# Kernel optimization log

Hardware: AMD Instinct MI355X
Metric: run time of the kernel (lower is better)

The kernel has to match this reference:

```python
import jax, jax.numpy as jnp
import numpy as np

N, A, D = 8192, 512, 512
NN = 3  # n_neighbors


def setup_inputs() -> dict:
    key = jax.random.key(0)
    ks = jax.random.split(key, 7)
    emb = jax.random.normal(ks[0], (N, D), jnp.float32)
    embedding = emb / jnp.linalg.norm(emb, axis=-1, keepdims=True)
    anc = jax.random.normal(ks[1], (A, D), jnp.float32)
    anchors = anc / jnp.linalg.norm(anc, axis=-1, keepdims=True)
    tri = 2.0 * jax.random.uniform(ks[2], (N, A), jnp.float32)  # 1 - cos in [0,2]
    # gate MLP params (Linear(3,16) -> GELU -> Linear(16,1)).
    # NOTE: original init zeros W2 / bias=2.0; random weights used here so the
    # reference exercises nontrivial compute. b2 kept at the module's +2.0.
    W1 = jax.random.normal(ks[3], (16, 3), jnp.float32) * 0.5
    b1 = jax.random.normal(ks[4], (16,), jnp.float32) * 0.1
    W2 = jax.random.normal(ks[5], (1, 16), jnp.float32) * 0.1
    b2 = jnp.full((1,), 2.0, jnp.float32)
    return {"embedding": embedding, "anchors": anchors, "tri": tri,
            "W1": W1, "b1": b1, "W2": W2, "b2": b2}


def _anchor_neighborhood_cm(anchors):
    # pairwise euclidean distances (A,A) with self excluded
    g = anchors @ anchors.T
    sq = jnp.diag(g)
    d2_full = jnp.maximum(sq[:, None] + sq[None, :] - 2.0 * g, 0.0)
    dists = jnp.sqrt(d2_full) + jnp.eye(A, dtype=anchors.dtype) * 1e12
    nn_idx = jnp.argsort(dists, axis=-1)[:, :NN]                       # (A, NN)
    simplices = jnp.concatenate([anchors[:, None, :], anchors[nn_idx]], axis=1)  # (A,K,D)
    K = NN + 1
    # batched pairwise squared distances within each simplex
    gram = jnp.einsum('aid,ajd->aij', simplices, simplices)            # (A,K,K)
    diag = jnp.diagonal(gram, axis1=-2, axis2=-1)
    d2 = diag[:, :, None] + diag[:, None, :] - 2.0 * gram
    # Cayley-Menger matrix (A, K+1, K+1)
    M = jnp.zeros((A, K + 1, K + 1), anchors.dtype)
    M = M.at[:, 0, 1:].set(1.0)
    M = M.at[:, 1:, 0].set(1.0)
    M = M.at[:, 1:, 1:].set(d2)
    raw = jnp.linalg.det(M)
    sign_corr = (-1.0) ** K  # k = K-1, sign = (-1)^(k+1); K=4 -> +1
    dets = sign_corr * raw
    quality = jnp.sign(dets) * jnp.log(jnp.abs(dets) + 1e-12)
    return quality


def reference(embedding, anchors, tri, W1, b1, W2, b2):
    n, a = tri.shape
    anchor_cm = _anchor_neighborhood_cm(anchors)                        # (A,)
    cm_std = jnp.maximum(jnp.std(anchor_cm, ddof=1), 1e-8)
    anchor_cm_norm = (anchor_cm - jnp.mean(anchor_cm)) / cm_std
    cos_sim = 1.0 - tri                                                 # (N,A)
    ranks = jnp.argsort(jnp.argsort(tri, axis=-1), axis=-1).astype(tri.dtype)
    ranks = ranks / max(a - 1, 1)
    feats = jnp.stack([jnp.broadcast_to(anchor_cm_norm[None, :], (n, a)),
                       cos_sim, ranks], axis=-1)                        # (N,A,3)
    h = jax.nn.gelu(jnp.einsum('nac,hc->nah', feats, W1) + b1, approximate=False)
    logits = jnp.einsum('nah,oh->nao', h, W2)[..., 0] + b2[0]           # (N,A)
    return jax.nn.sigmoid(logits)
```

## Files before the change

### kernel.cpp

```cpp
#include <hip/hip_runtime.h>
#include <hip/hip_bf16.h>
#include <math.h>

#define N_ 8192
#define A_ 512
#define D_ 512
#define NN_ 3
#define KPARTS 4

__device__ __forceinline__ float gelu_poly(float x) {
  const float u  = x * x;
  const float s  = fminf(u, 9.0f);
  float p = fmaf(-2.8012e-4f, s, 6.4615e-3f);
  p = fmaf(p, s, -6.1073e-2f);
  p = fmaf(p, s, 3.96693e-1f);
  p = p * s;
  const float ax   = fabsf(x);
  const float e    = fminf(p, 0.5f * ax);
  const float tail = fmaxf(ax - 3.0f, 0.0f);
  return fmaf(0.5f, x, fmaf(0.5f, tail, e));
}

__global__ __launch_bounds__(64) void sq_kernel(
    const float* __restrict__ anchors, float* __restrict__ sq) {
  const int i = blockIdx.x;
  const int l = threadIdx.x;
  const float4* a = reinterpret_cast<const float4*>(anchors + (size_t)i * D_);
  float s = 0.f;
  for (int k = l; k < D_ / 4; k += 64) {
    float4 v = a[k];
    s += v.x * v.x + v.y * v.y + v.z * v.z + v.w * v.w;
  }
#pragma unroll
  for (int d = 32; d > 0; d >>= 1) s += __shfl_down(s, d);
  if (l == 0) sq[i] = s;
}

__global__ __launch_bounds__(256) void gram_tiled_kernel(
    const float* __restrict__ anchors, float* __restrict__ G) {
  __shared__ float At[32][68];
  __shared__ float Bt[32][68];

  const int tx = threadIdx.x;
  const int ty = threadIdx.y;
  const int tid = ty * 16 + tx;
  const int i0 = blockIdx.y * 64;
  const int j0 = blockIdx.x * 64;
  const int z  = blockIdx.z;
  float* Gz = G + (size_t)z * A_ * A_;

  const int r0 = tid >> 3;
  const int c4 = tid & 7;

  float acc[4][4];
#pragma unroll
  for (int m = 0; m < 4; ++m)
#pragma unroll
    for (int n = 0; n < 4; ++n) acc[m][n] = 0.f;

  for (int kt = z * (16 / KPARTS); kt < (z + 1) * (16 / KPARTS); ++kt) {
    const int kb = kt * 32 + c4 * 4;
    float4 va = *reinterpret_cast<const float4*>(&anchors[(size_t)(i0 + r0) * D_ + kb]);
    float4 vb = *reinterpret_cast<const float4*>(&anchors[(size_t)(i0 + r0 + 32) * D_ + kb]);
    float4 wa = *reinterpret_cast<const float4*>(&anchors[(size_t)(j0 + r0) * D_ + kb]);
    float4 wb = *reinterpret_cast<const float4*>(&anchors[(size_t)(j0 + r0 + 32) * D_ + kb]);
    __syncthreads();
    const int kc = c4 * 4;
    At[kc + 0][r0] = va.x; At[kc + 1][r0] = va.y; At[kc + 2][r0] = va.z; At[kc + 3][r0] = va.w;
    At[kc + 0][r0 + 32] = vb.x; At[kc + 1][r0 + 32] = vb.y; At[kc + 2][r0 + 32] = vb.z; At[kc + 3][r0 + 32] = vb.w;
    Bt[kc + 0][r0] = wa.x; Bt[kc + 1][r0] = wa.y; Bt[kc + 2][r0] = wa.z; Bt[kc + 3][r0] = wa.w;
    Bt[kc + 0][r0 + 32] = wb.x; Bt[kc + 1][r0 + 32] = wb.y; Bt[kc + 2][r0 + 32] = wb.z; Bt[kc + 3][r0 + 32] = wb.w;
    __syncthreads();

#pragma unroll
    for (int kk = 0; kk < 32; ++kk) {
      float4 a = *reinterpret_cast<const float4*>(&At[kk][ty * 4]);
      float4 b = *reinterpret_cast<const float4*>(&Bt[kk][tx * 4]);
      acc[0][0] += a.x * b.x; acc[0][1] += a.x * b.y; acc[0][2] += a.x * b.z; acc[0][3] += a.x * b.w;
      acc[1][0] += a.y * b.x; acc[1][1] += a.y * b.y; acc[1][2] += a.y * b.z; acc[1][3] += a.y * b.w;
      acc[2][0] += a.z * b.x; acc[2][1] += a.z * b.y; acc[2][2] += a.z * b.z; acc[2][3] += a.z * b.w;
      acc[3][0] += a.w * b.x; acc[3][1] += a.w * b.y; acc[3][2] += a.w * b.z; acc[3][3] += a.w * b.w;
    }
  }

#pragma unroll
  for (int m = 0; m < 4; ++m) {
    float4 st;
    st.x = acc[m][0]; st.y = acc[m][1]; st.z = acc[m][2]; st.w = acc[m][3];
    *reinterpret_cast<float4*>(&Gz[(size_t)(i0 + ty * 4 + m) * A_ + j0 + tx * 4]) = st;
  }
}

__device__ __forceinline__ void lexmin(float& v, int& j, float ov, int oj) {
  if (ov < v || (ov == v && oj < j)) { v = ov; j = oj; }
}

__global__ __launch_bounds__(64) void nn_det_kernel(
    const float* __restrict__ G, const float* __restrict__ sq,
    float* __restrict__ quality) {
  __shared__ float d2s[16];
  const int i = blockIdx.x;
  const int l = threadIdx.x;
  const float sqi = sq[i];
  const int jb = l * 8;

  float gg[8] = {0.f, 0.f, 0.f, 0.f, 0.f, 0.f, 0.f, 0.f};
#pragma unroll
  for (int z = 0; z < KPARTS; ++z) {
    const float* Grow = G + (size_t)z * A_ * A_ + (size_t)i * A_;
    float4 g0 = *reinterpret_cast<const float4*>(&Grow[jb]);
    float4 g1 = *reinterpret_cast<const float4*>(&Grow[jb + 4]);
    gg[0] += g0.x; gg[1] += g0.y; gg[2] += g0.z; gg[3] += g0.w;
    gg[4] += g1.x; gg[5] += g1.y; gg[6] += g1.z; gg[7] += g1.w;
  }
  float4 s0 = *reinterpret_cast<const float4*>(&sq[jb]);
  float4 s1 = *reinterpret_cast<const float4*>(&sq[jb + 4]);
  float ss[8] = { s0.x, s0.y, s0.z, s0.w, s1.x, s1.y, s1.z, s1.w };

  float dist[8];
#pragma unroll
  for (int q = 0; q < 8; ++q) {
    float d2 = fmaxf(sqi + ss[q] - 2.f * gg[q], 0.f);
    float dd = sqrtf(d2);
    if (jb + q == i) dd += 1e12f;
    dist[q] = dd;
  }

  int nn[NN_];
#pragma unroll
  for (int r = 0; r < NN_; ++r) {
    float bv = 1e30f;
    int bi = 0x7fffffff;
#pragma unroll
    for (int q = 0; q < 8; ++q) lexmin(bv, bi, dist[q], jb + q);
#pragma unroll
    for (int d = 1; d < 64; d <<= 1) {
      float ov = __shfl_xor(bv, d);
      int oi = __shfl_xor(bi, d);
      lexmin(bv, bi, ov, oi);
    }
    nn[r] = bi;
#pragma unroll
    for (int q = 0; q < 8; ++q)
      if (jb + q == bi) dist[q] = 1e30f;
  }

  if (l < 16) {
    const int p = l >> 2, q = l & 3;
    const int pi = (p == 0) ? i : ((p == 1) ? nn[0] : ((p == 2) ? nn[1] : nn[2]));
    const int qi = (q == 0) ? i : ((q == 1) ? nn[0] : ((q == 2) ? nn[1] : nn[2]));
    float d2f;
    if (p == q) {
      d2f = 0.f;
    } else {
      float g = 0.f;
#pragma unroll
      for (int z = 0; z < KPARTS; ++z)
        g += G[(size_t)z * A_ * A_ + (size_t)pi * A_ + qi];
      d2f = sq[pi] + sq[qi] - 2.f * g;
    }
    d2s[l] = d2f;
  }
  __syncthreads();

  if (l == 0) {
    double M[5][5];
    M[0][0] = 0.0;
    for (int q = 1; q < 5; ++q) { M[0][q] = 1.0; M[q][0] = 1.0; }
    for (int p = 0; p < 4; ++p)
      for (int q = 0; q < 4; ++q)
        M[p + 1][q + 1] = (double)d2s[p * 4 + q];

    double det = 1.0;
    for (int c = 0; c < 5; ++c) {
      int piv = c;
      double mx = fabs(M[c][c]);
      for (int r2 = c + 1; r2 < 5; ++r2) {
        double v = fabs(M[r2][c]);
        if (v > mx) { mx = v; piv = r2; }
      }
      if (piv != c) {
        for (int c2 = 0; c2 < 5; ++c2) { double tmp = M[c][c2]; M[c][c2] = M[piv][c2]; M[piv][c2] = tmp; }
        det = -det;
      }
      double pv = M[c][c];
      det *= pv;
      if (pv == 0.0) break;
      for (int r2 = c + 1; r2 < 5; ++r2) {
        double f = M[r2][c] / pv;
        for (int c2 = c; c2 < 5; ++c2) M[r2][c2] -= f * M[c][c2];
      }
    }
    float raw = (float)det;
    float sg = (raw > 0.f) ? 1.f : ((raw < 0.f) ? -1.f : 0.f);
    quality[i] = sg * logf(fabsf(raw) + 1e-12f);
  }
}

__global__ __launch_bounds__(A_) void norm_cm_kernel(
    const float* __restrict__ quality, float* __restrict__ cmn) {
  __shared__ float red[A_];
  const int t = threadIdx.x;
  float q = quality[t];
  red[t] = q;
  __syncthreads();
  for (int s = A_ / 2; s > 0; s >>= 1) {
    if (t < s) red[t] += red[t + s];
    __syncthreads();
  }
  float mean = red[0] * (1.0f / A_);
  __syncthreads();
  float dq = q - mean;
  red[t] = dq * dq;
  __syncthreads();
  for (int s = A_ / 2; s > 0; s >>= 1) {
    if (t < s) red[t] += red[t + s];
    __syncthreads();
  }
  float sd = sqrtf(red[0] * (1.0f / (A_ - 1)));
  sd = fmaxf(sd, 1e-8f);
  cmn[t] = dq / sd;
}

__global__ __launch_bounds__(A_) void gate_fused(
    const float* __restrict__ tri, const float* __restrict__ cmn,
    const float* __restrict__ W1, const float* __restrict__ b1,
    const float* __restrict__ W2, const float* __restrict__ b2,
    float* __restrict__ out) {
  __shared__ int hist[256];
  __shared__ int pref[256];
  __shared__ int cursor[256];
  __shared__ unsigned long long sorted[A_];

  const int n = blockIdx.x;
  const int t = threadIdx.x;

  const float ti = tri[(size_t)n * A_ + t];
  const unsigned long long key =
      ((unsigned long long)__float_as_uint(ti) << 9) | (unsigned)t;
  int b = (int)(ti * 128.0f);
  b = (b < 0) ? 0 : ((b > 255) ? 255 : b);

  if (t < 256) { hist[t] = 0; cursor[t] = 0; }
  __syncthreads();
  atomicAdd(&hist[b], 1);
  __syncthreads();

  if (t < 64) {
    const int b4 = t * 4;
    int h0 = hist[b4 + 0], h1 = hist[b4 + 1], h2 = hist[b4 + 2], h3 = hist[b4 + 3];
    int s = h0 + h1 + h2 + h3;
    int incl = s;
#pragma unroll
    for (int d = 1; d < 64; d <<= 1) {
      int u = __shfl_up(incl, d);
      if (t >= d) incl += u;
    }
    int ex = incl - s;
    pref[b4 + 0] = ex;
    pref[b4 + 1] = ex + h0;
    pref[b4 + 2] = ex + h0 + h1;
    pref[b4 + 3] = ex + h0 + h1 + h2;
  }
  __syncthreads();

  const int pos = pref[b] + atomicAdd(&cursor[b], 1);
  sorted[pos] = key;
  __syncthreads();

  const int start = pref[b];
  const int len = hist[b];
  int cnt = start;
  for (int m = 0; m < len; ++m) cnt += (sorted[start + m] < key);
  const float rank = (float)cnt * (1.0f / (A_ - 1));

  const float f0 = cmn[t];
  const float f1 = 1.0f - ti;

  float logit = b2[0];
#pragma unroll
  for (int k = 0; k < 16; ++k) {
    float x = fmaf(W1[k * 3 + 0], f0,
              fmaf(W1[k * 3 + 1], f1,
              fmaf(W1[k * 3 + 2], rank, b1[k])));
    logit = fmaf(W2[k], gelu_poly(x), logit);
  }
  const float eneg = exp2f(logit * -1.44269504088896340736f);
  out[(size_t)n * A_ + t] = __builtin_amdgcn_rcpf(1.0f + eneg);
}

extern "C" void kernel_launch(void* const* d_in, const int* in_sizes, int n_in,
                              void* d_out, int out_size, void* d_ws, size_t ws_size,
                              hipStream_t stream) {
  const float* anchors = (const float*)d_in[1];
  const float* tri     = (const float*)d_in[2];
  const float* W1      = (const float*)d_in[3];
  const float* b1      = (const float*)d_in[4];
  const float* W2      = (const float*)d_in[5];
  const float* b2      = (const float*)d_in[6];
  float* out = (float*)d_out;

  float* G        = (float*)d_ws;
  float* sq       = G + (size_t)KPARTS * A_ * A_;
  float* quality  = sq + A_;
  float* cmn      = quality + A_;

  sq_kernel<<<A_, 64, 0, stream>>>(anchors, sq);
  gram_tiled_kernel<<<dim3(8, 8, KPARTS), dim3(16, 16), 0, stream>>>(anchors, G);
  nn_det_kernel<<<A_, 64, 0, stream>>>(G, sq, quality);
  norm_cm_kernel<<<1, A_, 0, stream>>>(quality, cmn);
  gate_fused<<<N_, A_, 0, stream>>>(tri, cmn, W1, b1, W2, b2, out);
}
```

Measured before the change: 63.47 us.

## Rank each row within a single wavefront and double gram K-split

The gate kernel now handles one row per 64-lane wavefront, with each lane owning eight elements. Loads and stores are vectorised to float4, and wave barriers replace block-wide __syncthreads in the bucket-sort ranking. Prefix offsets and counts are packed into one shared array, and the per-bucket cursor counts down on the histogram instead of using a separate array. This removes block-level synchronisation and cuts LDS arrays. KPARTS also goes from 4 to 8, so the gram kernel's reduction is split further. The trade-off is more serial work per thread, which may lose latency hiding.

```diff
diff --git a/kernel.cpp b/kernel.cpp
--- a/kernel.cpp
+++ b/kernel.cpp
@@ -6,7 +6,7 @@
 #define A_ 512
 #define D_ 512
 #define NN_ 3
-#define KPARTS 4
+#define KPARTS 8
 
 __device__ __forceinline__ float gelu_poly(float x) {
   const float u  = x * x;
@@ -222,71 +222,97 @@
   cmn[t] = dq / sd;
 }
 
-__global__ __launch_bounds__(A_) void gate_fused(
+__global__ __launch_bounds__(256) void gate_wave(
     const float* __restrict__ tri, const float* __restrict__ cmn,
     const float* __restrict__ W1, const float* __restrict__ b1,
     const float* __restrict__ W2, const float* __restrict__ b2,
     float* __restrict__ out) {
-  __shared__ int hist[256];
-  __shared__ int pref[256];
-  __shared__ int cursor[256];
-  __shared__ unsigned long long sorted[A_];
-
-  const int n = blockIdx.x;
-  const int t = threadIdx.x;
-
-  const float ti = tri[(size_t)n * A_ + t];
-  const unsigned long long key =
-      ((unsigned long long)__float_as_uint(ti) << 9) | (unsigned)t;
-  int b = (int)(ti * 128.0f);
-  b = (b < 0) ? 0 : ((b > 255) ? 255 : b);
-
-  if (t < 256) { hist[t] = 0; cursor[t] = 0; }
-  __syncthreads();
-  atomicAdd(&hist[b], 1);
-  __syncthreads();
-
-  if (t < 64) {
-    const int b4 = t * 4;
-    int h0 = hist[b4 + 0], h1 = hist[b4 + 1], h2 = hist[b4 + 2], h3 = hist[b4 + 3];
-    int s = h0 + h1 + h2 + h3;
-    int incl = s;
-#pragma unroll
-    for (int d = 1; d < 64; d <<= 1) {
-      int u = __shfl_up(incl, d);
-      if (t >= d) incl += u;
-    }
-    int ex = incl - s;
-    pref[b4 + 0] = ex;
-    pref[b4 + 1] = ex + h0;
-    pref[b4 + 2] = ex + h0 + h1;
-    pref[b4 + 3] = ex + h0 + h1 + h2;
-  }
-  __syncthreads();
-
-  const int pos = pref[b] + atomicAdd(&cursor[b], 1);
-  sorted[pos] = key;
-  __syncthreads();
-
-  const int start = pref[b];
-  const int len = hist[b];
-  int cnt = start;
-  for (int m = 0; m < len; ++m) cnt += (sorted[start + m] < key);
-  const float rank = (float)cnt * (1.0f / (A_ - 1));
-
-  const float f0 = cmn[t];
-  const float f1 = 1.0f - ti;
-
-  float logit = b2[0];
-#pragma unroll
-  for (int k = 0; k < 16; ++k) {
-    float x = fmaf(W1[k * 3 + 0], f0,
-              fmaf(W1[k * 3 + 1], f1,
-              fmaf(W1[k * 3 + 2], rank, b1[k])));
-    logit = fmaf(W2[k], gelu_poly(x), logit);
-  }
-  const float eneg = exp2f(logit * -1.44269504088896340736f);
-  out[(size_t)n * A_ + t] = __builtin_amdgcn_rcpf(1.0f + eneg);
+  __shared__ int hist[4][256];
+  __shared__ int pk[4][256];
+  __shared__ unsigned long long sorted[4][A_];
+
+  const int w = threadIdx.x >> 6;
+  const int l = threadIdx.x & 63;
+  const int n = blockIdx.x * 4 + w;
+  const size_t rowo = (size_t)n * A_;
+  const int e0 = l * 8;
+
+  float4 tv0 = *reinterpret_cast<const float4*>(tri + rowo + e0);
+  float4 tv1 = *reinterpret_cast<const float4*>(tri + rowo + e0 + 4);
+  const float ti[8] = { tv0.x, tv0.y, tv0.z, tv0.w, tv1.x, tv1.y, tv1.z, tv1.w };
+
+  int4 z4; z4.x = 0; z4.y = 0; z4.z = 0; z4.w = 0;
+  *reinterpret_cast<int4*>(&hist[w][l * 4]) = z4;
+  __builtin_amdgcn_wave_barrier();
+
+  unsigned long long key[8];
+  int bb[8];
+#pragma unroll
+  for (int q = 0; q < 8; ++q) {
+    key[q] = ((unsigned long long)__float_as_uint(ti[q]) << 9) | (unsigned)(e0 + q);
+    int b = (int)(ti[q] * 128.0f);
+    bb[q] = (b < 0) ? 0 : ((b > 255) ? 255 : b);
+    atomicAdd(&hist[w][bb[q]], 1);
+  }
+  __builtin_amdgcn_wave_barrier();
+
+  int4 h4 = *reinterpret_cast<const int4*>(&hist[w][l * 4]);
+  const int s = h4.x + h4.y + h4.z + h4.w;
+  int incl = s;
+#pragma unroll
+  for (int d = 1; d < 64; d <<= 1) {
+    int u = __shfl_up(incl, d);
+    if (l >= d) incl += u;
+  }
+  const int ex = incl - s;
+  int4 pkv;
+  pkv.x = (ex << 16) | h4.x;
+  pkv.y = ((ex + h4.x) << 16) | h4.y;
+  pkv.z = ((ex + h4.x + h4.y) << 16) | h4.z;
+  pkv.w = ((ex + h4.x + h4.y + h4.z) << 16) | h4.w;
+  *reinterpret_cast<int4*>(&pk[w][l * 4]) = pkv;
+  __builtin_amdgcn_wave_barrier();
+
+  int start[8], len[8];
+#pragma unroll
+  for (int q = 0; q < 8; ++q) {
+    const int p = pk[w][bb[q]];
+    start[q] = p >> 16;
+    len[q]   = p & 0xffff;
+    const int pos = start[q] + atomicAdd(&hist[w][bb[q]], -1) - 1;
+    sorted[w][pos] = key[q];
+  }
+  __builtin_amdgcn_wave_barrier();
+
+  float4 cv0 = *reinterpret_cast<const float4*>(cmn + e0);
+  float4 cv1 = *reinterpret_cast<const float4*>(cmn + e0 + 4);
+  const float f0a[8] = { cv0.x, cv0.y, cv0.z, cv0.w, cv1.x, cv1.y, cv1.z, cv1.w };
+
+  float res[8];
+#pragma unroll
+  for (int q = 0; q < 8; ++q) {
+    int cnt = start[q];
+    for (int m = 0; m < len[q]; ++m) cnt += (sorted[w][start[q] + m] < key[q]);
+    const float rank = (float)cnt * (1.0f / (A_ - 1));
+    const float f0 = f0a[q];
+    const float f1 = 1.0f - ti[q];
+
+    float logit = b2[0];
+#pragma unroll
+    for (int k = 0; k < 16; ++k) {
+      float x = fmaf(W1[k * 3 + 0], f0,
+                fmaf(W1[k * 3 + 1], f1,
+                fmaf(W1[k * 3 + 2], rank, b1[k])));
+      logit = fmaf(W2[k], gelu_poly(x), logit);
+    }
+    res[q] = __builtin_amdgcn_rcpf(1.0f + exp2f(logit * -1.44269504088896340736f));
+  }
+
+  float4 o0, o1;
+  o0.x = res[0]; o0.y = res[1]; o0.z = res[2]; o0.w = res[3];
+  o1.x = res[4]; o1.y = res[5]; o1.z = res[6]; o1.w = res[7];
+  *reinterpret_cast<float4*>(out + rowo + e0)     = o0;
+  *reinterpret_cast<float4*>(out + rowo + e0 + 4) = o1;
 }
 
 extern "C" void kernel_launch(void* const* d_in, const int* in_sizes, int n_in,
@@ -309,5 +335,5 @@
   gram_tiled_kernel<<<dim3(8, 8, KPARTS), dim3(16, 16), 0, stream>>>(anchors, G);
   nn_det_kernel<<<A_, 64, 0, stream>>>(G, sq, quality);
   norm_cm_kernel<<<1, A_, 0, stream>>>(quality, cmn);
-  gate_fused<<<N_, A_, 0, stream>>>(tri, cmn, W1, b1, W2, b2, out);
-}
+  gate_wave<<<N_ / 4, 256, 0, stream>>>(tri, cmn, W1, b1, W2, b2, out);
+}
```

New measurement: 70.20 us. 10.6% more time.

## Evaluate gate MLP hidden layer in packed fp16 and raise Gram K-split

Applied to the files above, without the earlier changes.

Moves the 16-unit gate MLP hidden layer and its GELU polynomial to packed half2 arithmetic, processing two hidden units per instruction. W1 and b1 are pre-packed into fp16 pairs by an extra block of the sq kernel. KPARTS is also raised from 4 to 8, splitting the Gram matrix reduction further. The aim is to halve the ALU instruction count in the main per-element gate kernel, at the cost of fp16 precision in the features and activations, which may breach tolerance.

```diff
diff --git a/kernel.cpp b/kernel.cpp
--- a/kernel.cpp
+++ b/kernel.cpp
@@ -6,25 +6,27 @@
 #define A_ 512
 #define D_ 512
 #define NN_ 3
-#define KPARTS 4
-
-__device__ __forceinline__ float gelu_poly(float x) {
-  const float u  = x * x;
-  const float s  = fminf(u, 9.0f);
-  float p = fmaf(-2.8012e-4f, s, 6.4615e-3f);
-  p = fmaf(p, s, -6.1073e-2f);
-  p = fmaf(p, s, 3.96693e-1f);
-  p = p * s;
-  const float ax   = fabsf(x);
-  const float e    = fminf(p, 0.5f * ax);
-  const float tail = fmaxf(ax - 3.0f, 0.0f);
-  return fmaf(0.5f, x, fmaf(0.5f, tail, e));
-}
+#define KPARTS 8
+
+typedef _Float16 h2 __attribute__((ext_vector_type(2)));
 
 __global__ __launch_bounds__(64) void sq_kernel(
-    const float* __restrict__ anchors, float* __restrict__ sq) {
+    const float* __restrict__ anchors, float* __restrict__ sq,
+    const float* __restrict__ W1, const float* __restrict__ b1,
+    h2* __restrict__ wpk) {
   const int i = blockIdx.x;
   const int l = threadIdx.x;
+  if (i == A_) {
+    if (l < 8) {
+      h2 a, b, c, d;
+      a.x = (_Float16)W1[(2 * l) * 3 + 0]; a.y = (_Float16)W1[(2 * l + 1) * 3 + 0];
+      b.x = (_Float16)W1[(2 * l) * 3 + 1]; b.y = (_Float16)W1[(2 * l + 1) * 3 + 1];
+      c.x = (_Float16)W1[(2 * l) * 3 + 2]; c.y = (_Float16)W1[(2 * l + 1) * 3 + 2];
+      d.x = (_Float16)b1[2 * l];           d.y = (_Float16)b1[2 * l + 1];
+      wpk[l] = a; wpk[8 + l] = b; wpk[16 + l] = c; wpk[24 + l] = d;
+    }
+    return;
+  }
   const float4* a = reinterpret_cast<const float4*>(anchors + (size_t)i * D_);
   float s = 0.f;
   for (int k = l; k < D_ / 4; k += 64) {
@@ -224,7 +226,7 @@
 
 __global__ __launch_bounds__(A_) void gate_fused(
     const float* __restrict__ tri, const float* __restrict__ cmn,
-    const float* __restrict__ W1, const float* __restrict__ b1,
+    const h2* __restrict__ wpk,
     const float* __restrict__ W2, const float* __restrict__ b2,
     float* __restrict__ out) {
   __shared__ int hist[256];
@@ -248,8 +250,8 @@
 
   if (t < 64) {
     const int b4 = t * 4;
-    int h0 = hist[b4 + 0], h1 = hist[b4 + 1], h2 = hist[b4 + 2], h3 = hist[b4 + 3];
-    int s = h0 + h1 + h2 + h3;
+    int h0 = hist[b4 + 0], h1 = hist[b4 + 1], h2v = hist[b4 + 2], h3 = hist[b4 + 3];
+    int s = h0 + h1 + h2v + h3;
     int incl = s;
 #pragma unroll
     for (int d = 1; d < 64; d <<= 1) {
@@ -260,7 +262,7 @@
     pref[b4 + 0] = ex;
     pref[b4 + 1] = ex + h0;
     pref[b4 + 2] = ex + h0 + h1;
-    pref[b4 + 3] = ex + h0 + h1 + h2;
+    pref[b4 + 3] = ex + h0 + h1 + h2v;
   }
   __syncthreads();
 
@@ -277,13 +279,35 @@
   const float f0 = cmn[t];
   const float f1 = 1.0f - ti;
 
+  h2 f0h; f0h.x = (_Float16)f0;   f0h.y = f0h.x;
+  h2 f1h; f1h.x = (_Float16)f1;   f1h.y = f1h.x;
+  h2 rkh; rkh.x = (_Float16)rank; rkh.y = rkh.x;
+
+  h2 nine2;  nine2.x = (_Float16)9.0f;  nine2.y = nine2.x;
+  h2 three2; three2.x = (_Float16)3.0f; three2.y = three2.x;
+  h2 zero2;  zero2.x = (_Float16)0.0f;  zero2.y = zero2.x;
+  h2 cA; cA.x = (_Float16)(-2.8012e-4f);  cA.y = cA.x;
+  h2 cB; cB.x = (_Float16)(6.4615e-3f);   cB.y = cB.x;
+  h2 cC; cC.x = (_Float16)(-6.1073e-2f);  cC.y = cC.x;
+  h2 cD; cD.x = (_Float16)(3.96693e-1f);  cD.y = cD.x;
+  h2 hf; hf.x = (_Float16)0.5f; hf.y = hf.x;
+
   float logit = b2[0];
 #pragma unroll
-  for (int k = 0; k < 16; ++k) {
-    float x = fmaf(W1[k * 3 + 0], f0,
-              fmaf(W1[k * 3 + 1], f1,
-              fmaf(W1[k * 3 + 2], rank, b1[k])));
-    logit = fmaf(W2[k], gelu_poly(x), logit);
+  for (int kp = 0; kp < 8; ++kp) {
+    h2 x = wpk[kp] * f0h + (wpk[8 + kp] * f1h + (wpk[16 + kp] * rkh + wpk[24 + kp]));
+    h2 u = x * x;
+    h2 s = __builtin_elementwise_min(u, nine2);
+    h2 p = cA * s + cB;
+    p = p * s + cC;
+    p = p * s + cD;
+    p = p * s;
+    h2 ax = __builtin_elementwise_abs(x);
+    h2 e = __builtin_elementwise_min(p, hf * ax);
+    h2 tail = __builtin_elementwise_max(ax - three2, zero2);
+    h2 g = hf * x + (hf * tail + e);
+    logit = fmaf(W2[2 * kp],     (float)g.x, logit);
+    logit = fmaf(W2[2 * kp + 1], (float)g.y, logit);
   }
   const float eneg = exp2f(logit * -1.44269504088896340736f);
   out[(size_t)n * A_ + t] = __builtin_amdgcn_rcpf(1.0f + eneg);
@@ -304,10 +328,11 @@
   float* sq       = G + (size_t)KPARTS * A_ * A_;
   float* quality  = sq + A_;
   float* cmn      = quality + A_;
-
-  sq_kernel<<<A_, 64, 0, stream>>>(anchors, sq);
+  h2* wpk         = (h2*)(cmn + A_);
+
+  sq_kernel<<<A_ + 1, 64, 0, stream>>>(anchors, sq, W1, b1, wpk);
   gram_tiled_kernel<<<dim3(8, 8, KPARTS), dim3(16, 16), 0, stream>>>(anchors, G);
   nn_det_kernel<<<A_, 64, 0, stream>>>(G, sq, quality);
   norm_cm_kernel<<<1, A_, 0, stream>>>(quality, cmn);
-  gate_fused<<<N_, A_, 0, stream>>>(tri, cmn, W1, b1, W2, b2, out);
-}
+  gate_fused<<<N_, A_, 0, stream>>>(tri, cmn, wpk, W2, b2, out);
+}
```

New measurement: 59.88 us. -5.7%, faster.
